# Optimization experiments

Hardware: AMD Instinct MI355X
Metric: run time of the kernel (lower is better)

## Reference

```python
import jax, jax.numpy as jnp
import numpy as np

B, L, D = 4, 2048, 1024
DK, H = 64, 16
DFF = 4 * D
MASK_FILL = -2**15 + 1  # -32767, matches masked_fill value in source


def setup_inputs() -> dict:
    key = jax.random.key(0)
    ks = jax.random.split(key, 16)
    s = lambda fan_in: 1.0 / np.sqrt(fan_in)
    inp = {
        "x": jax.random.normal(ks[0], (B, L, D), dtype=jnp.float32),
        "maskPAD": jax.random.randint(ks[1], (B, L, L), 0, 2, dtype=jnp.int32),
        # attention projections (torch Linear layout: [out, in])
        "WQ_w": jax.random.uniform(ks[2], (H * DK, D), jnp.float32, -s(D), s(D)),
        "WQ_b": jnp.zeros((H * DK,), jnp.float32),
        "WK_w": jax.random.uniform(ks[3], (H * DK, D), jnp.float32, -s(D), s(D)),
        "WK_b": jnp.zeros((H * DK,), jnp.float32),
        "WV_w": jax.random.uniform(ks[4], (H * DK, D), jnp.float32, -s(D), s(D)),
        "WV_b": jnp.zeros((H * DK,), jnp.float32),
        "WO_w": jax.random.uniform(ks[5], (D, H * DK), jnp.float32, -s(H * DK), s(H * DK)),
        "WO_b": jnp.zeros((D,), jnp.float32),
        # FFN (pre-LN inside the FFN block)
        "ln_g": jnp.ones((D,), jnp.float32),
        "ln_b": jnp.zeros((D,), jnp.float32),
        "W1_w": jax.random.uniform(ks[6], (DFF, D), jnp.float32, -s(D), s(D)),
        "W1_b": jnp.zeros((DFF,), jnp.float32),
        "W2_w": jax.random.uniform(ks[7], (D, DFF), jnp.float32, -s(DFF), s(DFF)),
        "W2_b": jnp.zeros((D,), jnp.float32),
    }
    return inp


def _layernorm(x, g, b, eps=1e-5):
    mu = jnp.mean(x, axis=-1, keepdims=True)
    var = jnp.var(x, axis=-1, keepdims=True)
    return (x - mu) * jax.lax.rsqrt(var + eps) * g + b


def reference(x, maskPAD, WQ_w, WQ_b, WK_w, WK_b, WV_w, WV_b, WO_w, WO_b,
              ln_g, ln_b, W1_w, W1_b, W2_w, W2_b):
    # --- SelfAttention_PostLN (dropout = identity at eval) ---
    q = (jnp.einsum('bld,ed->ble', x, WQ_w) + WQ_b).reshape(B, L, H, DK).transpose(0, 2, 1, 3)
    k = (jnp.einsum('bld,ed->ble', x, WK_w) + WK_b).reshape(B, L, H, DK).transpose(0, 2, 1, 3)
    v = (jnp.einsum('bld,ed->ble', x, WV_w) + WV_b).reshape(B, L, H, DK).transpose(0, 2, 1, 3)
    scores = jnp.einsum('bhqd,bhkd->bhqk', q, k) / np.sqrt(DK).astype(np.float32)
    scores = jnp.where((maskPAD == 0)[:, None, :, :], jnp.float32(MASK_FILL), scores)
    alpha = jax.nn.softmax(scores, axis=-1)
    z = jnp.einsum('bhqk,bhkd->bhqd', alpha, v)  # [B,H,L,DK]
    z = z.transpose(0, 2, 1, 3).reshape(B, L, H * DK)
    z = jnp.einsum('ble,de->bld', z, WO_w) + WO_b
    # --- FFN_PreLN ---
    r = x + z                                    # residual 1 (dropout identity)
    h = _layernorm(r, ln_g, ln_b)
    h = jax.nn.relu(jnp.einsum('bld,fd->blf', h, W1_w) + W1_b)
    h = jnp.einsum('blf,df->bld', h, W2_w) + W2_b
    return r + h
```

## Files before the change

kernel.cpp:

```cpp
#include <hip/hip_runtime.h>

#define BD      4
#define LSEQ    2048
#define DMODEL  1024
#define HHEADS  16
#define DKK     64
#define DFFN    4096
#define MROWS   (BD*LSEQ)
#define QKVS    3072

typedef float  f32x4  __attribute__((ext_vector_type(4)));
typedef float  f32x16 __attribute__((ext_vector_type(16)));
typedef __bf16 bf16x8 __attribute__((ext_vector_type(8)));
typedef unsigned short u16x8 __attribute__((ext_vector_type(8)));
typedef unsigned int   u32x4 __attribute__((ext_vector_type(4)));

__device__ inline unsigned short f2bf(float x) {
    union { float f; unsigned u; } c; c.f = x;
    unsigned r = c.u + 0x7FFFu + ((c.u >> 16) & 1u);
    return (unsigned short)(r >> 16);
}

__global__ void cast_bf16_k(const float* __restrict__ in,
                            unsigned short* __restrict__ out, long n) {
    long i = ((long)blockIdx.x * blockDim.x + threadIdx.x) * 4;
    long stride = (long)gridDim.x * blockDim.x * 4;
    for (; i < n; i += stride) {
        float4 v = *(const float4*)(in + i);
        ushort4 o;
        o.x = f2bf(v.x); o.y = f2bf(v.y); o.z = f2bf(v.z); o.w = f2bf(v.w);
        *(ushort4*)(out + i) = o;
    }
}

__global__ void concat3_k(const float* __restrict__ a, const float* __restrict__ b,
                          const float* __restrict__ c, float* __restrict__ o) {
    int i = blockIdx.x * 256 + threadIdx.x;
    if (i < 1024) { o[i] = a[i]; o[1024 + i] = b[i]; o[2048 + i] = c[i]; }
}

__global__ __launch_bounds__(256) void maskbits_k(const int* __restrict__ m,
                                                  unsigned long long* __restrict__ bits) {
    const long gw = ((long)blockIdx.x * blockDim.x + threadIdx.x) >> 6;
    const int lane = threadIdx.x & 63;
    const int b   = (int)(gw >> 16);
    const int rem = (int)gw & 65535;
    const int q = rem >> 5, kt = rem & 31;
    const int v = m[((size_t)(b*LSEQ + q))*LSEQ + kt*64 + lane];
    const unsigned long long bal = __ballot(v != 0);
    if (lane == 0) bits[((size_t)(b*32 + kt))*LSEQ + q] = bal;
}

__device__ inline void gload16(const void* g, void* l) {
    __builtin_amdgcn_global_load_lds(
        (const __attribute__((address_space(1))) void*)g,
        (__attribute__((address_space(3))) void*)l, 16, 0, 0);
}

#define BAR() { __builtin_amdgcn_sched_barrier(0); __builtin_amdgcn_s_barrier(); __builtin_amdgcn_sched_barrier(0); }

#define STAGE(XSEL, XPTR, h, tau, s)                                              \
  { const unsigned short* gs0 = (XPTR) + (size_t)((h)*128 + wid*8 + srow) * K + (tau)*64 + schk*8; \
    gload16(gs0, (void*)&sm[(s)][(XSEL)][(((h)*128 + wid*8)*64)]);                 \
    gload16(gs0 + (size_t)64*K, (void*)&sm[(s)][(XSEL)][(((h)*128 + 64 + wid*8)*64)]); }

#define LDA(dst, s, mi, kk) dst = *(const bf16x8*)(&sm[(s)][0][(wr*128 + (mi)*16 + r0)*64 + ((((kk)*4 + g) ^ (r0 & 7)) << 3)]);
#define LDB(dst, s, nj, kk) dst = *(const bf16x8*)(&sm[(s)][1][(wc*64  + (nj)*16 + r0)*64 + ((((kk)*4 + g) ^ (r0 & 7)) << 3)]);

#define PHASE_MFMA(q)                                                                                   \
    __builtin_amdgcn_s_setprio(1);                                                                      \
    _Pragma("unroll")                                                                                   \
    for (int nj = 0; nj < 4; ++nj) {                                                                    \
        acc[2*(q)][nj]   = __builtin_amdgcn_mfma_f32_16x16x32_bf16(af00, bq[nj][0], acc[2*(q)][nj],   0,0,0); \
        acc[2*(q)][nj]   = __builtin_amdgcn_mfma_f32_16x16x32_bf16(af01, bq[nj][1], acc[2*(q)][nj],   0,0,0); \
        acc[2*(q)+1][nj] = __builtin_amdgcn_mfma_f32_16x16x32_bf16(af10, bq[nj][0], acc[2*(q)+1][nj], 0,0,0); \
        acc[2*(q)+1][nj] = __builtin_amdgcn_mfma_f32_16x16x32_bf16(af11, bq[nj][1], acc[2*(q)+1][nj], 0,0,0); \
    }                                                                                                   \
    __builtin_amdgcn_s_setprio(0);

#define KTILE(s, tau)                                                        \
  {                                                                          \
    const int tp1 = (tau) + 1, tp2 = (tau) + 2;                              \
    bf16x8 bq[4][2];                                                         \
    bf16x8 af00, af01, af10, af11;                                           \
    _Pragma("unroll") for (int nj = 0; nj < 4; ++nj) {                       \
        LDB(bq[nj][0], s, nj, 0); LDB(bq[nj][1], s, nj, 1); }                \
    LDA(af00, s, 0, 0); LDA(af01, s, 0, 1);                                  \
    LDA(af10, s, 1, 0); LDA(af11, s, 1, 1);                                  \
    if (tp1 < NTT) { STAGE(0, Ab, 0, tp1, (s)^1); }                          \
    BAR(); PHASE_MFMA(0); BAR();                                             \
    LDA(af00, s, 2, 0); LDA(af01, s, 2, 1);                                  \
    LDA(af10, s, 3, 0); LDA(af11, s, 3, 1);                                  \
    if (tp1 < NTT) { STAGE(0, Ab, 1, tp1, (s)^1); }                          \
    if (tp2 < NTT) { STAGE(1, Bb, 0, tp2, (s)); }                            \
    BAR(); PHASE_MFMA(1); BAR();                                             \
    LDA(af00, s, 4, 0); LDA(af01, s, 4, 1);                                  \
    LDA(af10, s, 5, 0); LDA(af11, s, 5, 1);                                  \
    if (tp2 < NTT) { STAGE(1, Bb, 1, tp2, (s)); }                            \
    BAR(); PHASE_MFMA(2); BAR();                                             \
    LDA(af00, s, 6, 0); LDA(af01, s, 6, 1);                                  \
    LDA(af10, s, 7, 0); LDA(af11, s, 7, 1);                                  \
    if (tp2 < NTT)      { asm volatile("s_waitcnt vmcnt(4)" ::: "memory"); } \
    else if (tp1 < NTT) { asm volatile("s_waitcnt vmcnt(0)" ::: "memory"); } \
    BAR(); PHASE_MFMA(3); BAR();                                             \
  }

template<int MODE, int NTT>
__global__ __launch_bounds__(512, 1) void gemm8(const unsigned short* __restrict__ A,
                                                const unsigned short* __restrict__ B,
                                                const float* __restrict__ bias,
                                                unsigned short* __restrict__ Cout,
                                                int M, int N, int K, float scaleQ)
{
    __shared__ unsigned short sm[2][2][256*64];
    const int t   = threadIdx.x;
    const int wid = t >> 6, lane = t & 63;
    const int wr  = wid >> 2, wc = wid & 3;
    const int r0  = lane & 15, g = lane >> 4;

    const int nwg = gridDim.x;
    const int bid = (blockIdx.x & 7) * (nwg >> 3) + (blockIdx.x >> 3);
    const int ntn = N >> 8;
    const int bm  = (bid / ntn) << 8, bn = (bid % ntn) << 8;

    const int srow = lane >> 3;
    const int schk = (lane & 7) ^ srow;
    const unsigned short* Ab = A + (size_t)bm * K;
    const unsigned short* Bb = B + (size_t)bn * K;

    f32x4 acc[8][4] = {};

    STAGE(1, Bb, 0, 0, 0); STAGE(1, Bb, 1, 0, 0);
    STAGE(0, Ab, 0, 0, 0); STAGE(0, Ab, 1, 0, 0);
    STAGE(1, Bb, 0, 1, 1); STAGE(1, Bb, 1, 1, 1);
    asm volatile("s_waitcnt vmcnt(4)" ::: "memory");
    BAR();

#pragma unroll 1
    for (int i2 = 0; i2 < NTT/2; ++i2) {
        const int tau = 2*i2;
        KTILE(0, tau);
        KTILE(1, tau+1);
    }

#pragma unroll
    for (int mi = 0; mi < 8; ++mi) {
        const int row0 = bm + wr*128 + mi*16 + g*4;
#pragma unroll
        for (int nj = 0; nj < 4; ++nj) {
            const int col = bn + wc*64 + nj*16 + r0;
            const float bcol = bias[col];
            const float sc = (MODE == 0) ? (col < 1024 ? scaleQ : 1.0f) : 1.0f;
#pragma unroll
            for (int rr = 0; rr < 4; ++rr) {
                float c = (acc[mi][nj][rr] + bcol) * sc;
                if (MODE == 1) c = fmaxf(c, 0.f);
                Cout[(size_t)(row0 + rr) * N + col] = f2bf(c);
            }
        }
    }
}

#define STAGEA2(h, tau, s)                                                        \
  { const unsigned short* gs0 = Ab + (size_t)((h)*128 + wid*8 + srow) * K + (tau)*64 + schk*8; \
    gload16(gs0, (void*)&smA[(s)][(((h)*128 + wid*8)*64)]);                        \
    gload16(gs0 + (size_t)64*K, (void*)&smA[(s)][(((h)*128 + 64 + wid*8)*64)]); }

#define STAGEB2(tau, s)                                                           \
  { const unsigned short* gs0 = Bb + (size_t)(wid*8 + srow) * K + (tau)*64 + schk*8; \
    gload16(gs0, (void*)&smB[(s)][((wid*8)*64)]);                                  \
    gload16(gs0 + (size_t)64*K, (void*)&smB[(s)][((64 + wid*8)*64)]); }

#define LDA2(dst, s, mi, kk) dst = *(const bf16x8*)(&smA[(s)][(wr*128 + (mi)*16 + r0)*64 + ((((kk)*4 + g) ^ (r0 & 7)) << 3)]);
#define LDB2(dst, s, nj, kk) dst = *(const bf16x8*)(&smB[(s)][(wc*32  + (nj)*16 + r0)*64 + ((((kk)*4 + g) ^ (r0 & 7)) << 3)]);

#define PHASE_MFMA2(q)                                                                                  \
    __builtin_amdgcn_s_setprio(1);                                                                      \
    _Pragma("unroll")                                                                                   \
    for (int nj = 0; nj < 2; ++nj) {                                                                    \
        acc[2*(q)][nj]   = __builtin_amdgcn_mfma_f32_16x16x32_bf16(af00, bq[nj][0], acc[2*(q)][nj],   0,0,0); \
        acc[2*(q)][nj]   = __builtin_amdgcn_mfma_f32_16x16x32_bf16(af01, bq[nj][1], acc[2*(q)][nj],   0,0,0); \
        acc[2*(q)+1][nj] = __builtin_amdgcn_mfma_f32_16x16x32_bf16(af10, bq[nj][0], acc[2*(q)+1][nj], 0,0,0); \
        acc[2*(q)+1][nj] = __builtin_amdgcn_mfma_f32_16x16x32_bf16(af11, bq[nj][1], acc[2*(q)+1][nj], 0,0,0); \
    }                                                                                                   \
    __builtin_amdgcn_s_setprio(0);

#define KTILE2(s, tau)                                                       \
  {                                                                          \
    const int tp1 = (tau) + 1, tp2 = (tau) + 2;                              \
    bf16x8 bq[2][2];                                                         \
    bf16x8 af00, af01, af10, af11;                                           \
    _Pragma("unroll") for (int nj = 0; nj < 2; ++nj) {                       \
        LDB2(bq[nj][0], s, nj, 0); LDB2(bq[nj][1], s, nj, 1); }              \
    LDA2(af00, s, 0, 0); LDA2(af01, s, 0, 1);                                \
    LDA2(af10, s, 1, 0); LDA2(af11, s, 1, 1);                                \
    if (tp1 < NTT) { STAGEA2(0, tp1, (s)^1); }                               \
    BAR(); PHASE_MFMA2(0); BAR();                                            \
    LDA2(af00, s, 2, 0); LDA2(af01, s, 2, 1);                                \
    LDA2(af10, s, 3, 0); LDA2(af11, s, 3, 1);                                \
    if (tp1 < NTT) { STAGEA2(1, tp1, (s)^1); }                               \
    BAR(); PHASE_MFMA2(1); BAR();                                            \
    LDA2(af00, s, 4, 0); LDA2(af01, s, 4, 1);                                \
    LDA2(af10, s, 5, 0); LDA2(af11, s, 5, 1);                                \
    if (tp2 < NTT) { STAGEB2(tp2, (s)); }                                    \
    BAR(); PHASE_MFMA2(2); BAR();                                            \
    LDA2(af00, s, 6, 0); LDA2(af01, s, 6, 1);                                \
    LDA2(af10, s, 7, 0); LDA2(af11, s, 7, 1);                                \
    if (tp2 < NTT)      { asm volatile("s_waitcnt vmcnt(2)" ::: "memory"); } \
    else if (tp1 < NTT) { asm volatile("s_waitcnt vmcnt(0)" ::: "memory"); } \
    BAR(); PHASE_MFMA2(3); BAR();                                            \
  }

template<int MODE, int NTT>
__global__ __launch_bounds__(512, 1) void gemm8n(const unsigned short* __restrict__ A,
                                                 const unsigned short* __restrict__ B,
                                                 const float* __restrict__ bias,
                                                 const float* __restrict__ resid,
                                                 void* __restrict__ Cout,
                                                 int M, int N, int K, float scaleQ)
{
    __shared__ unsigned short smA[2][256*64];
    __shared__ unsigned short smB[2][128*64];
    const int t   = threadIdx.x;
    const int wid = t >> 6, lane = t & 63;
    const int wr  = wid >> 2, wc = wid & 3;
    const int r0  = lane & 15, g = lane >> 4;

    const int nwg = gridDim.x;
    const int bid = (blockIdx.x & 7) * (nwg >> 3) + (blockIdx.x >> 3);
    const int ntn = N >> 7;
    const int bm  = (bid / ntn) << 8, bn = (bid % ntn) << 7;

    const int srow = lane >> 3;
    const int schk = (lane & 7) ^ srow;
    const unsigned short* Ab = A + (size_t)bm * K;
    const unsigned short* Bb = B + (size_t)bn * K;

    f32x4 acc[8][2] = {};

    STAGEB2(0, 0);
    STAGEA2(0, 0, 0); STAGEA2(1, 0, 0);
    STAGEB2(1, 1);
    asm volatile("s_waitcnt vmcnt(2)" ::: "memory");
    BAR();

#pragma unroll 1
    for (int i2 = 0; i2 < NTT/2; ++i2) {
        const int tau = 2*i2;
        KTILE2(0, tau);
        KTILE2(1, tau+1);
    }

#pragma unroll
    for (int mi = 0; mi < 8; ++mi) {
        const int row0 = bm + wr*128 + mi*16 + g*4;
#pragma unroll
        for (int nj = 0; nj < 2; ++nj) {
            const int col = bn + wc*32 + nj*16 + r0;
            const float bcol = bias[col];
            const float sc = (MODE == 0) ? (col < 1024 ? scaleQ : 1.0f) : 1.0f;
#pragma unroll
            for (int rr = 0; rr < 4; ++rr) {
                const int row = row0 + rr;
                float c = (acc[mi][nj][rr] + bcol) * sc;
                if (MODE == 2) {
                    ((float*)Cout)[(size_t)row * N + col] = c + resid[(size_t)row * N + col];
                } else {
                    ((unsigned short*)Cout)[(size_t)row * N + col] = f2bf(c);
                }
            }
        }
    }
}

template<int MODE>
__global__ __launch_bounds__(256) void gemm_nt(const unsigned short* __restrict__ A,
                                               const unsigned short* __restrict__ B,
                                               const float* __restrict__ bias,
                                               const float* __restrict__ resid,
                                               void* __restrict__ Cout,
                                               int M, int N, int K, float scale)
{
    __shared__ unsigned short As[128*32];
    __shared__ unsigned short Bs[128*32];
    const int t    = threadIdx.x;
    const int w    = t >> 6, lane = t & 63;
    const int r0   = lane & 15, g = lane >> 4;
    const int wm   = (w >> 1) * 64, wn = (w & 1) * 64;
    const int bm   = blockIdx.y * 128, bn = blockIdx.x * 128;
    const int srow = t >> 2, scol = (t & 3) * 8;

    const unsigned short* Ag = A + (size_t)(bm + srow) * K + scol;
    const unsigned short* Bg = B + (size_t)(bn + srow) * K + scol;
    unsigned short* AsW = As + w * 512;
    unsigned short* BsW = Bs + w * 512;

    f32x4 acc[4][4] = {};

    for (int kt = 0; kt < K; kt += 32) {
        gload16(Ag + kt,                AsW);
        gload16(Ag + (size_t)64*K + kt, AsW + 2048);
        gload16(Bg + kt,                BsW);
        gload16(Bg + (size_t)64*K + kt, BsW + 2048);
        __syncthreads();
        bf16x8 af[4], bfr[4];
#pragma unroll
        for (int i = 0; i < 4; ++i)
            af[i] = *(const bf16x8*)(As + (wm + i*16 + r0)*32 + g*8);
#pragma unroll
        for (int j = 0; j < 4; ++j)
            bfr[j] = *(const bf16x8*)(Bs + (wn + j*16 + r0)*32 + g*8);
#pragma unroll
        for (int i = 0; i < 4; ++i)
#pragma unroll
            for (int j = 0; j < 4; ++j)
                acc[i][j] = __builtin_amdgcn_mfma_f32_16x16x32_bf16(af[i], bfr[j], acc[i][j], 0, 0, 0);
        __syncthreads();
    }

#pragma unroll
    for (int i = 0; i < 4; ++i) {
        const int row0 = bm + wm + i*16 + g*4;
#pragma unroll
        for (int j = 0; j < 4; ++j) {
            const int col = bn + wn + j*16 + r0;
            const float bcol = bias[col];
#pragma unroll
            for (int rr = 0; rr < 4; ++rr) {
                const int row = row0 + rr;
                float c = (acc[i][j][rr] + bcol) * scale;
                if (MODE == 2) {
                    ((float*)Cout)[(size_t)row * N + col] = c + resid[(size_t)row * N + col];
                } else {
                    if (MODE == 1) c = fmaxf(c, 0.f);
                    ((unsigned short*)Cout)[(size_t)row * N + col] = f2bf(c);
                }
            }
        }
    }
}

#define MFILL   (-47272.79f)
#define DEFTHR  (11.5415603f)
__global__ __launch_bounds__(256) void attn_k(
    const unsigned short* __restrict__ QKV,
    const unsigned long long* __restrict__ MBits,
    unsigned short* __restrict__ Z)
{
    __shared__ unsigned short Ks[2][64*64];
    __shared__ unsigned short Vt[2][64*64];
    __shared__ unsigned short Qs[128*64];
    __shared__ float Sc[4*32];

    const int t    = threadIdx.x;
    const int w    = t >> 6, lane = t & 63;
    const int q31  = lane & 31, hi = lane >> 5;

    const int bid = blockIdx.x;
    const int sw  = (bid & 7) * 128 + (bid >> 3);
    const int qt  = sw & 15, h = (sw >> 4) & 15, b = sw >> 8;
    const int qw  = qt * 128 + w * 32;

    {
        const int qrow = t & 127;
        const int cb   = (t >> 7) * 4;
        const unsigned short* Qgs = QKV + ((size_t)(b*LSEQ + qt*128 + qrow))*QKVS + h*DKK;
#pragma unroll
        for (int j = 0; j < 4; ++j) {
            u16x8 qv = *(const u16x8*)(Qgs + (cb + j)*8);
            *(u16x8*)&Qs[qrow*64 + (((cb + j) ^ (qrow & 7)) << 3)] = qv;
        }
    }

    const int krow  = w*8 + (lane>>3);
    const int kchk  = (lane & 7) ^ (krow & 7);
    const unsigned short* Kg = QKV + ((size_t)(b*LSEQ))*QKVS + 1024 + h*DKK;
    const int kp   = w*8 + (lane>>3);
    const int vd0  = (lane & 7) * 8;
    const unsigned short* Vg = QKV + ((size_t)(b*LSEQ))*QKVS + 2048 + h*DKK + vd0;
    const unsigned short* Qrow = &Qs[(w*32 + q31)*64];

    float m_r = MFILL, l_r = 0.f;
    f32x16 z0, z1;
#pragma unroll
    for (int r = 0; r < 16; ++r) { z0[r] = 0.f; z1[r] = 0.f; }

    {
        u16x8 vA = *(const u16x8*)(Vg + (size_t)(kp*2)*QKVS);
        u16x8 vB = *(const u16x8*)(Vg + (size_t)(kp*2+1)*QKVS);
#pragma unroll
        for (int i = 0; i < 8; ++i) {
            const int d = vd0 + i;
            const int c = (kp>>2) ^ (d&7) ^ (d>>3);
            *(unsigned*)&Vt[0][d*64 + c*8 + 2*(kp&3)] = (unsigned)vA[i] | ((unsigned)vB[i] << 16);
        }
    }
    gload16(Kg + (size_t)krow*QKVS      + kchk*8, &Ks[0][w*512]);
    gload16(Kg + (size_t)(32+krow)*QKVS + kchk*8, &Ks[0][w*512] + 2048);
    unsigned long long mw = MBits[((size_t)(b*32 + 0))*LSEQ + (qw + q31)];

    __syncthreads();

    for (int kt = 0; kt < LSEQ/64; ++kt) {
        const int cur = kt & 1;
        const int ktn = (kt < LSEQ/64 - 1) ? kt + 1 : kt;
        const int k0n = ktn * 64;

        gload16(Kg + (size_t)(k0n + krow)*QKVS      + kchk*8, &Ks[cur^1][w*512]);
        gload16(Kg + (size_t)(k0n + 32 + krow)*QKVS + kchk*8, &Ks[cur^1][w*512] + 2048);
        u16x8 vA = *(const u16x8*)(Vg + (size_t)(k0n + kp*2)*QKVS);
        u16x8 vB = *(const u16x8*)(Vg + (size_t)(k0n + kp*2+1)*QKVS);
        const unsigned long long mwn = MBits[((size_t)(b*32 + ktn))*LSEQ + (qw + q31)];

        const unsigned long long sh = mw >> (hi*4);
        const unsigned md0 = (unsigned)sh, md1 = (unsigned)(sh >> 32);

        f32x16 s0, s1;
#pragma unroll
        for (int r = 0; r < 16; ++r) { s0[r] = 0.f; s1[r] = 0.f; }
        __builtin_amdgcn_s_setprio(1);
#pragma unroll
        for (int ds = 0; ds < 4; ++ds) {
            const int slot = ((ds*2 + hi) ^ (q31 & 7)) << 3;
            bf16x8 kf0 = *(const bf16x8*)(&Ks[cur][ q31     *64 + slot]);
            bf16x8 kf1 = *(const bf16x8*)(&Ks[cur][(32+q31)*64 + slot]);
            bf16x8 qf  = *(const bf16x8*)(Qrow + slot);
            s0 = __builtin_amdgcn_mfma_f32_32x32x16_bf16(kf0, qf, s0, 0, 0, 0);
            s1 = __builtin_amdgcn_mfma_f32_32x32x16_bf16(kf1, qf, s1, 0, 0, 0);
        }
        __builtin_amdgcn_s_setprio(0);

#pragma unroll
        for (int r = 0; r < 16; ++r) {
            const int kb = (r & 3) + 8*(r >> 2);
            if (!((md0 >> kb) & 1)) s0[r] = MFILL;
            if (!((md1 >> kb) & 1)) s1[r] = MFILL;
        }

        float tm = fmaxf(s0[0], s1[0]);
#pragma unroll
        for (int r = 1; r < 16; ++r) tm = fmaxf(tm, fmaxf(s0[r], s1[r]));
        {
            float ta = tm, tb = tm;
            asm volatile("v_permlane32_swap_b32 %0, %1" : "+v"(ta), "+v"(tb));
            tm = fmaxf(tm, hi ? ta : tb);
        }

        if (__any(tm > m_r + DEFTHR)) {
            const float nm   = fmaxf(m_r, tm);
            const float corr = exp2f(m_r - nm);
            Sc[w*32 + q31] = corr;
            l_r *= corr;
            m_r  = nm;
#pragma unroll
            for (int r = 0; r < 16; ++r) {
                const int row = (r & 3) + 8*(r >> 2) + 4*hi;
                const float cr = Sc[w*32 + row];
                z0[r] *= cr; z1[r] *= cr;
            }
        }

#pragma unroll
        for (int r = 0; r < 16; ++r) {
            s0[r] = exp2f(s0[r] - m_r);
            s1[r] = exp2f(s1[r] - m_r);
        }
        float r4[8];
#pragma unroll
        for (int r = 0; r < 8; ++r)
            r4[r] = (s0[2*r] + s0[2*r+1]) + (s1[2*r] + s1[2*r+1]);
        float rs = ((r4[0]+r4[1]) + (r4[2]+r4[3])) + ((r4[4]+r4[5]) + (r4[6]+r4[7]));
        {
            float ra = rs, rb = rs;
            asm volatile("v_permlane32_swap_b32 %0, %1" : "+v"(ra), "+v"(rb));
            rs += hi ? ra : rb;
        }
        l_r += rs;

        __builtin_amdgcn_s_setprio(1);
#pragma unroll
        for (int half = 0; half < 2; ++half) {
#pragma unroll
            for (int sub = 0; sub < 2; ++sub) {
                const int base = sub*8;
                unsigned wa, wb, wc2, wd;
                float p0 = half ? s1[base+0] : s0[base+0];
                float p1 = half ? s1[base+1] : s0[base+1];
                float p2 = half ? s1[base+2] : s0[base+2];
                float p3 = half ? s1[base+3] : s0[base+3];
                float p4 = half ? s1[base+4] : s0[base+4];
                float p5 = half ? s1[base+5] : s0[base+5];
                float p6 = half ? s1[base+6] : s0[base+6];
                float p7 = half ? s1[base+7] : s0[base+7];
                asm("v_cvt_pk_bf16_f32 %0, %1, %2" : "=v"(wa) : "v"(p0), "v"(p1));
                asm("v_cvt_pk_bf16_f32 %0, %1, %2" : "=v"(wb) : "v"(p4), "v"(p5));
                asm("v_cvt_pk_bf16_f32 %0, %1, %2" : "=v"(wc2) : "v"(p2), "v"(p3));
                asm("v_cvt_pk_bf16_f32 %0, %1, %2" : "=v"(wd) : "v"(p6), "v"(p7));
                asm volatile("v_permlane32_swap_b32 %0, %1" : "+v"(wa), "+v"(wb));
                asm volatile("v_permlane32_swap_b32 %0, %1" : "+v"(wc2), "+v"(wd));
                u32x4 pu; pu[0] = wa; pu[1] = wc2; pu[2] = wb; pu[3] = wd;
                bf16x8 pa = __builtin_bit_cast(bf16x8, pu);
                const int ks = half*2 + sub;
                const int ch = ks*2 + hi;
                bf16x8 vf0 = *(const bf16x8*)(&Vt[cur][ q31     *64 + ((ch ^ (q31&7) ^ ( q31>>3)     ) << 3)]);
                bf16x8 vf1 = *(const bf16x8*)(&Vt[cur][(32+q31)*64 + ((ch ^ (q31&7) ^ ((32+q31)>>3)) << 3)]);
                z0 = __builtin_amdgcn_mfma_f32_32x32x16_bf16(pa, vf0, z0, 0, 0, 0);
                z1 = __builtin_amdgcn_mfma_f32_32x32x16_bf16(pa, vf1, z1, 0, 0, 0);
            }
        }
        __builtin_amdgcn_s_setprio(0);

#pragma unroll
        for (int i = 0; i < 8; ++i) {
            const int d = vd0 + i;
            const int c = (kp>>2) ^ (d&7) ^ (d>>3);
            *(unsigned*)&Vt[cur^1][d*64 + c*8 + 2*(kp&3)] = (unsigned)vA[i] | ((unsigned)vB[i] << 16);
        }
        mw = mwn;
        __syncthreads();
    }

    Sc[w*32 + q31] = l_r;
    unsigned short* Zb = Z + ((size_t)(b*LSEQ + qw))*DMODEL + h*DKK + q31;
#pragma unroll
    for (int r = 0; r < 16; ++r) {
        const int row = (r & 3) + 8*(r >> 2) + 4*hi;
        const float rl = 1.0f / Sc[w*32 + row];
        Zb[(size_t)row*DMODEL]      = f2bf(z0[r] * rl);
        Zb[(size_t)row*DMODEL + 32] = f2bf(z1[r] * rl);
    }
}

__global__ __launch_bounds__(256) void ln_k(const float* __restrict__ r,
                                            const float* __restrict__ gam,
                                            const float* __restrict__ bet,
                                            unsigned short* __restrict__ out)
{
    const int row = blockIdx.x;
    const int t = threadIdx.x;
    const float* rp = r + (size_t)row * DMODEL;
    float4 v = *(const float4*)(rp + t*4);
    float s  = v.x + v.y + v.z + v.w;
    float s2 = v.x*v.x + v.y*v.y + v.z*v.z + v.w*v.w;
#pragma unroll
    for (int off = 32; off >= 1; off >>= 1) {
        s  += __shfl_xor(s,  off);
        s2 += __shfl_xor(s2, off);
    }
    __shared__ float red[8];
    const int wv = t >> 6;
    if ((t & 63) == 0) { red[wv] = s; red[4 + wv] = s2; }
    __syncthreads();
    s  = red[0] + red[1] + red[2] + red[3];
    s2 = red[4] + red[5] + red[6] + red[7];
    const float mu   = s  * (1.f/DMODEL);
    const float var  = s2 * (1.f/DMODEL) - mu*mu;
    const float rstd = rsqrtf(var + 1e-5f);
    float4 gv = *(const float4*)(gam + t*4);
    float4 bv = *(const float4*)(bet + t*4);
    ushort4 o;
    o.x = f2bf((v.x - mu)*rstd*gv.x + bv.x);
    o.y = f2bf((v.y - mu)*rstd*gv.y + bv.y);
    o.z = f2bf((v.z - mu)*rstd*gv.z + bv.z);
    o.w = f2bf((v.w - mu)*rstd*gv.w + bv.w);
    *(ushort4*)(out + (size_t)row * DMODEL + t*4) = o;
}

extern "C" void kernel_launch(void* const* d_in, const int* in_sizes, int n_in,
                              void* d_out, int out_size, void* d_ws, size_t ws_size,
                              hipStream_t stream)
{
    const float* x    = (const float*)d_in[0];
    const int*   mask = (const int*)  d_in[1];
    const float* WQ_w = (const float*)d_in[2];
    const float* WQ_b = (const float*)d_in[3];
    const float* WK_w = (const float*)d_in[4];
    const float* WK_b = (const float*)d_in[5];
    const float* WV_w = (const float*)d_in[6];
    const float* WV_b = (const float*)d_in[7];
    const float* WO_w = (const float*)d_in[8];
    const float* WO_b = (const float*)d_in[9];
    const float* ln_g = (const float*)d_in[10];
    const float* ln_b = (const float*)d_in[11];
    const float* W1_w = (const float*)d_in[12];
    const float* W1_b = (const float*)d_in[13];
    const float* W2_w = (const float*)d_in[14];
    const float* W2_b = (const float*)d_in[15];
    float* out = (float*)d_out;

    char* w = (char*)d_ws;
    const size_t MB = 1024*1024;
    unsigned short* qkv  = (unsigned short*)(w + 0*MB);
    unsigned short* Zb   = (unsigned short*)(w + 48*MB);
    unsigned short* xb   = (unsigned short*)(w + 64*MB);
    float*          rb   = (float*)         (w + 80*MB);
    unsigned short* wqkv = (unsigned short*)(w + 112*MB);
    unsigned short* wob  = (unsigned short*)(w + 118*MB);
    unsigned short* w1b  = (unsigned short*)(w + 120*MB);
    unsigned short* w2b  = (unsigned short*)(w + 128*MB);
    unsigned long long* mbits = (unsigned long long*)(w + 136*MB);
    float* bqkv = (float*)(w + 48*MB);
    unsigned short* hln  = xb;
    unsigned short* hmid = (unsigned short*)(w + 0*MB);

    cast_bf16_k<<<2048, 256, 0, stream>>>(x,    xb,   (long)MROWS*DMODEL);
    cast_bf16_k<<<512,  256, 0, stream>>>(WQ_w, wqkv,               (long)DMODEL*DMODEL);
    cast_bf16_k<<<512,  256, 0, stream>>>(WK_w, wqkv + 1024*1024,   (long)DMODEL*DMODEL);
    cast_bf16_k<<<512,  256, 0, stream>>>(WV_w, wqkv + 2*1024*1024, (long)DMODEL*DMODEL);
    cast_bf16_k<<<512,  256, 0, stream>>>(WO_w, wob,  (long)DMODEL*DMODEL);
    cast_bf16_k<<<2048, 256, 0, stream>>>(W1_w, w1b,  (long)DFFN*DMODEL);
    cast_bf16_k<<<2048, 256, 0, stream>>>(W2_w, w2b,  (long)DMODEL*DFFN);
    maskbits_k<<<65536, 256, 0, stream>>>(mask, mbits);
    concat3_k<<<4, 256, 0, stream>>>(WQ_b, WK_b, WV_b, bqkv);

    gemm8n<0, 16><<<dim3(768), dim3(512), 0, stream>>>(xb, wqkv, bqkv, nullptr, qkv,
                                                       MROWS, QKVS, DMODEL, 0.18033688f);
    attn_k<<<dim3(1024), dim3(256), 0, stream>>>(qkv, mbits, Zb);
    gemm_nt<2><<<dim3(8, 64), dim3(256), 0, stream>>>(Zb, wob, WO_b, x, rb, MROWS, DMODEL, DMODEL, 1.0f);
    ln_k<<<MROWS, 256, 0, stream>>>(rb, ln_g, ln_b, hln);
    gemm8<1, 16><<<dim3(512), dim3(512), 0, stream>>>(hln, w1b, W1_b, hmid,
                                                      MROWS, DFFN, DMODEL, 1.0f);
    gemm8n<2, 64><<<dim3(256), dim3(512), 0, stream>>>(hmid, w2b, W2_b, rb, out,
                                                       MROWS, DMODEL, DFFN, 1.0f);
}
```

Before: 508.2 us.

## Emit V transposed from QKV GEMM and stream Q from registers in attention

The QKV projection GEMM now writes Q and K to a 2048-wide buffer and V transposed per batch/dim into a separate buffer. Attention can then load V tiles with async global-to-LDS copies instead of register loads plus a scalar transpose-and-pack into LDS. Q fragments are held in registers instead of being staged through shared memory, and the loop barrier moves to the start of each iteration. In exchange the GEMM epilogue does strided 8-byte transposed stores, and several workspace buffers now alias one another, which depends on the kernel ordering staying the same.

```diff
diff --git a/kernel.cpp b/kernel.cpp
--- a/kernel.cpp
+++ b/kernel.cpp
@@ -7,7 +7,7 @@
 #define DKK     64
 #define DFFN    4096
 #define MROWS   (BD*LSEQ)
-#define QKVS    3072
+#define QKS     2048
 
 typedef float  f32x4  __attribute__((ext_vector_type(4)));
 typedef float  f32x16 __attribute__((ext_vector_type(16)));
@@ -150,10 +150,9 @@
         for (int nj = 0; nj < 4; ++nj) {
             const int col = bn + wc*64 + nj*16 + r0;
             const float bcol = bias[col];
-            const float sc = (MODE == 0) ? (col < 1024 ? scaleQ : 1.0f) : 1.0f;
 #pragma unroll
             for (int rr = 0; rr < 4; ++rr) {
-                float c = (acc[mi][nj][rr] + bcol) * sc;
+                float c = acc[mi][nj][rr] + bcol;
                 if (MODE == 1) c = fmaxf(c, 0.f);
                 Cout[(size_t)(row0 + rr) * N + col] = f2bf(c);
             }
@@ -217,6 +216,7 @@
                                                  const float* __restrict__ bias,
                                                  const float* __restrict__ resid,
                                                  void* __restrict__ Cout,
+                                                 unsigned short* __restrict__ vt,
                                                  int M, int N, int K, float scaleQ)
 {
     __shared__ unsigned short smA[2][256*64];
@@ -258,15 +258,30 @@
         for (int nj = 0; nj < 2; ++nj) {
             const int col = bn + wc*32 + nj*16 + r0;
             const float bcol = bias[col];
-            const float sc = (MODE == 0) ? (col < 1024 ? scaleQ : 1.0f) : 1.0f;
 #pragma unroll
             for (int rr = 0; rr < 4; ++rr) {
                 const int row = row0 + rr;
-                float c = (acc[mi][nj][rr] + bcol) * sc;
                 if (MODE == 2) {
+                    float c = acc[mi][nj][rr] + bcol;
                     ((float*)Cout)[(size_t)row * N + col] = c + resid[(size_t)row * N + col];
+                }
+            }
+            if (MODE == 3) {
+                if (col < 2048) {
+                    const float sc = (col < 1024) ? scaleQ : 1.0f;
+#pragma unroll
+                    for (int rr = 0; rr < 4; ++rr)
+                        ((unsigned short*)Cout)[(size_t)(row0 + rr) * QKS + col] =
+                            f2bf((acc[mi][nj][rr] + bcol) * sc);
                 } else {
-                    ((unsigned short*)Cout)[(size_t)row * N + col] = f2bf(c);
+                    const int vcol = col - 2048;
+                    const int b = row0 >> 11, tok = row0 & 2047;
+                    ushort4 h4;
+                    h4.x = f2bf(acc[mi][nj][0] + bcol);
+                    h4.y = f2bf(acc[mi][nj][1] + bcol);
+                    h4.z = f2bf(acc[mi][nj][2] + bcol);
+                    h4.w = f2bf(acc[mi][nj][3] + bcol);
+                    *(ushort4*)&vt[((size_t)(b*1024 + vcol))*LSEQ + tok] = h4;
                 }
             }
         }
@@ -343,13 +358,13 @@
 #define MFILL   (-47272.79f)
 #define DEFTHR  (11.5415603f)
 __global__ __launch_bounds__(256) void attn_k(
-    const unsigned short* __restrict__ QKV,
+    const unsigned short* __restrict__ QK,
+    const unsigned short* __restrict__ VT,
     const unsigned long long* __restrict__ MBits,
     unsigned short* __restrict__ Z)
 {
     __shared__ unsigned short Ks[2][64*64];
-    __shared__ unsigned short Vt[2][64*64];
-    __shared__ unsigned short Qs[128*64];
+    __shared__ unsigned short Vs[2][64*64];
     __shared__ float Sc[4*32];
 
     const int t    = threadIdx.x;
@@ -361,55 +376,38 @@
     const int qt  = sw & 15, h = (sw >> 4) & 15, b = sw >> 8;
     const int qw  = qt * 128 + w * 32;
 
-    {
-        const int qrow = t & 127;
-        const int cb   = (t >> 7) * 4;
-        const unsigned short* Qgs = QKV + ((size_t)(b*LSEQ + qt*128 + qrow))*QKVS + h*DKK;
-#pragma unroll
-        for (int j = 0; j < 4; ++j) {
-            u16x8 qv = *(const u16x8*)(Qgs + (cb + j)*8);
-            *(u16x8*)&Qs[qrow*64 + (((cb + j) ^ (qrow & 7)) << 3)] = qv;
-        }
-    }
-
-    const int krow  = w*8 + (lane>>3);
-    const int kchk  = (lane & 7) ^ (krow & 7);
-    const unsigned short* Kg = QKV + ((size_t)(b*LSEQ))*QKVS + 1024 + h*DKK;
-    const int kp   = w*8 + (lane>>3);
-    const int vd0  = (lane & 7) * 8;
-    const unsigned short* Vg = QKV + ((size_t)(b*LSEQ))*QKVS + 2048 + h*DKK + vd0;
-    const unsigned short* Qrow = &Qs[(w*32 + q31)*64];
+    const unsigned short* Qg = QK + ((size_t)(b*LSEQ + qw + q31))*QKS + h*DKK + hi*8;
+    bf16x8 qf[4];
+#pragma unroll
+    for (int ds = 0; ds < 4; ++ds)
+        qf[ds] = *(const bf16x8*)(Qg + ds*16);
+
+    const int srow = w*8 + (lane>>3);
+    const int schk = (lane & 7) ^ (srow & 7);
+    const unsigned short* Kg = QK + ((size_t)(b*LSEQ))*QKS + 1024 + h*DKK;
+    const unsigned short* Vg = VT + ((size_t)(b*1024 + h*DKK))*LSEQ;
 
     float m_r = MFILL, l_r = 0.f;
     f32x16 z0, z1;
 #pragma unroll
     for (int r = 0; r < 16; ++r) { z0[r] = 0.f; z1[r] = 0.f; }
 
-    {
-        u16x8 vA = *(const u16x8*)(Vg + (size_t)(kp*2)*QKVS);
-        u16x8 vB = *(const u16x8*)(Vg + (size_t)(kp*2+1)*QKVS);
-#pragma unroll
-        for (int i = 0; i < 8; ++i) {
-            const int d = vd0 + i;
-            const int c = (kp>>2) ^ (d&7) ^ (d>>3);
-            *(unsigned*)&Vt[0][d*64 + c*8 + 2*(kp&3)] = (unsigned)vA[i] | ((unsigned)vB[i] << 16);
-        }
-    }
-    gload16(Kg + (size_t)krow*QKVS      + kchk*8, &Ks[0][w*512]);
-    gload16(Kg + (size_t)(32+krow)*QKVS + kchk*8, &Ks[0][w*512] + 2048);
+    gload16(Kg + (size_t)srow*QKS      + schk*8, &Ks[0][w*512]);
+    gload16(Kg + (size_t)(32+srow)*QKS + schk*8, &Ks[0][w*512] + 2048);
+    gload16(Vg + (size_t)srow*LSEQ      + schk*8, &Vs[0][w*512]);
+    gload16(Vg + (size_t)(32+srow)*LSEQ + schk*8, &Vs[0][w*512] + 2048);
     unsigned long long mw = MBits[((size_t)(b*32 + 0))*LSEQ + (qw + q31)];
-
-    __syncthreads();
 
     for (int kt = 0; kt < LSEQ/64; ++kt) {
         const int cur = kt & 1;
+        __syncthreads();
+
         const int ktn = (kt < LSEQ/64 - 1) ? kt + 1 : kt;
         const int k0n = ktn * 64;
-
-        gload16(Kg + (size_t)(k0n + krow)*QKVS      + kchk*8, &Ks[cur^1][w*512]);
-        gload16(Kg + (size_t)(k0n + 32 + krow)*QKVS + kchk*8, &Ks[cur^1][w*512] + 2048);
-        u16x8 vA = *(const u16x8*)(Vg + (size_t)(k0n + kp*2)*QKVS);
-        u16x8 vB = *(const u16x8*)(Vg + (size_t)(k0n + kp*2+1)*QKVS);
+        gload16(Kg + (size_t)(k0n + srow)*QKS      + schk*8, &Ks[cur^1][w*512]);
+        gload16(Kg + (size_t)(k0n + 32 + srow)*QKS + schk*8, &Ks[cur^1][w*512] + 2048);
+        gload16(Vg + (size_t)srow*LSEQ      + k0n + schk*8, &Vs[cur^1][w*512]);
+        gload16(Vg + (size_t)(32+srow)*LSEQ + k0n + schk*8, &Vs[cur^1][w*512] + 2048);
         const unsigned long long mwn = MBits[((size_t)(b*32 + ktn))*LSEQ + (qw + q31)];
 
         const unsigned long long sh = mw >> (hi*4);
@@ -424,9 +422,8 @@
             const int slot = ((ds*2 + hi) ^ (q31 & 7)) << 3;
             bf16x8 kf0 = *(const bf16x8*)(&Ks[cur][ q31     *64 + slot]);
             bf16x8 kf1 = *(const bf16x8*)(&Ks[cur][(32+q31)*64 + slot]);
-            bf16x8 qf  = *(const bf16x8*)(Qrow + slot);
-            s0 = __builtin_amdgcn_mfma_f32_32x32x16_bf16(kf0, qf, s0, 0, 0, 0);
-            s1 = __builtin_amdgcn_mfma_f32_32x32x16_bf16(kf1, qf, s1, 0, 0, 0);
+            s0 = __builtin_amdgcn_mfma_f32_32x32x16_bf16(kf0, qf[ds], s0, 0, 0, 0);
+            s1 = __builtin_amdgcn_mfma_f32_32x32x16_bf16(kf1, qf[ds], s1, 0, 0, 0);
         }
         __builtin_amdgcn_s_setprio(0);
 
@@ -501,23 +498,16 @@
                 u32x4 pu; pu[0] = wa; pu[1] = wc2; pu[2] = wb; pu[3] = wd;
                 bf16x8 pa = __builtin_bit_cast(bf16x8, pu);
                 const int ks = half*2 + sub;
-                const int ch = ks*2 + hi;
-                bf16x8 vf0 = *(const bf16x8*)(&Vt[cur][ q31     *64 + ((ch ^ (q31&7) ^ ( q31>>3)     ) << 3)]);
-                bf16x8 vf1 = *(const bf16x8*)(&Vt[cur][(32+q31)*64 + ((ch ^ (q31&7) ^ ((32+q31)>>3)) << 3)]);
+                const int slot = ((ks*2 + hi) ^ (q31 & 7)) << 3;
+                bf16x8 vf0 = *(const bf16x8*)(&Vs[cur][ q31     *64 + slot]);
+                bf16x8 vf1 = *(const bf16x8*)(&Vs[cur][(32+q31)*64 + slot]);
                 z0 = __builtin_amdgcn_mfma_f32_32x32x16_bf16(pa, vf0, z0, 0, 0, 0);
                 z1 = __builtin_amdgcn_mfma_f32_32x32x16_bf16(pa, vf1, z1, 0, 0, 0);
             }
         }
         __builtin_amdgcn_s_setprio(0);
 
-#pragma unroll
-        for (int i = 0; i < 8; ++i) {
-            const int d = vd0 + i;
-            const int c = (kp>>2) ^ (d&7) ^ (d>>3);
-            *(unsigned*)&Vt[cur^1][d*64 + c*8 + 2*(kp&3)] = (unsigned)vA[i] | ((unsigned)vB[i] << 16);
-        }
         mw = mwn;
-        __syncthreads();
     }
 
     Sc[w*32 + q31] = l_r;
@@ -590,17 +580,19 @@
 
     char* w = (char*)d_ws;
     const size_t MB = 1024*1024;
-    unsigned short* qkv  = (unsigned short*)(w + 0*MB);
-    unsigned short* Zb   = (unsigned short*)(w + 48*MB);
-    unsigned short* xb   = (unsigned short*)(w + 64*MB);
+    unsigned short* qk   = (unsigned short*)(w + 0*MB);
+    unsigned short* vtb  = (unsigned short*)(w + 32*MB);
+    unsigned short* shr  = (unsigned short*)(w + 64*MB);
     float*          rb   = (float*)         (w + 80*MB);
     unsigned short* wqkv = (unsigned short*)(w + 112*MB);
     unsigned short* wob  = (unsigned short*)(w + 118*MB);
     unsigned short* w1b  = (unsigned short*)(w + 120*MB);
     unsigned short* w2b  = (unsigned short*)(w + 128*MB);
     unsigned long long* mbits = (unsigned long long*)(w + 136*MB);
-    float* bqkv = (float*)(w + 48*MB);
-    unsigned short* hln  = xb;
+    float* bqkv = (float*)rb;
+    unsigned short* xb   = shr;
+    unsigned short* Zb   = shr;
+    unsigned short* hln  = shr;
     unsigned short* hmid = (unsigned short*)(w + 0*MB);
 
     cast_bf16_k<<<2048, 256, 0, stream>>>(x,    xb,   (long)MROWS*DMODEL);
@@ -613,13 +605,13 @@
     maskbits_k<<<65536, 256, 0, stream>>>(mask, mbits);
     concat3_k<<<4, 256, 0, stream>>>(WQ_b, WK_b, WV_b, bqkv);
 
-    gemm8n<0, 16><<<dim3(768), dim3(512), 0, stream>>>(xb, wqkv, bqkv, nullptr, qkv,
-                                                       MROWS, QKVS, DMODEL, 0.18033688f);
-    attn_k<<<dim3(1024), dim3(256), 0, stream>>>(qkv, mbits, Zb);
+    gemm8n<3, 16><<<dim3(768), dim3(512), 0, stream>>>(xb, wqkv, bqkv, nullptr, qk, vtb,
+                                                       MROWS, 3072, DMODEL, 0.18033688f);
+    attn_k<<<dim3(1024), dim3(256), 0, stream>>>(qk, vtb, mbits, Zb);
     gemm_nt<2><<<dim3(8, 64), dim3(256), 0, stream>>>(Zb, wob, WO_b, x, rb, MROWS, DMODEL, DMODEL, 1.0f);
     ln_k<<<MROWS, 256, 0, stream>>>(rb, ln_g, ln_b, hln);
     gemm8<1, 16><<<dim3(512), dim3(512), 0, stream>>>(hln, w1b, W1_b, hmid,
                                                       MROWS, DFFN, DMODEL, 1.0f);
-    gemm8n<2, 64><<<dim3(256), dim3(512), 0, stream>>>(hmid, w2b, W2_b, rb, out,
+    gemm8n<2, 64><<<dim3(256), dim3(512), 0, stream>>>(hmid, w2b, W2_b, rb, out, nullptr,
                                                        MROWS, DMODEL, DFFN, 1.0f);
 }
```

Result: faster. 485.2 us (-4.5%).
